# Kernel tuning notes

Hardware: AMD Instinct MI355X
Metric: run time of the kernel (lower is better)

## Reference

```python
import jax, jax.numpy as jnp
import numpy as np


def setup_inputs() -> dict:
    key = jax.random.key(0)
    ks = jax.random.split(key, 5)
    B, S, H = 4, 4096, 512
    std = 1.0 / np.sqrt(H)
    x = jax.random.normal(ks[0], (B, S, H), dtype=jnp.float32)
    relative_pos = jax.random.normal(ks[1], (B, S, H), dtype=jnp.float32)
    Wq = jax.random.normal(ks[2], (H, H), dtype=jnp.float32) * std
    Wk = jax.random.normal(ks[3], (H, H), dtype=jnp.float32) * std
    Wv = jax.random.normal(ks[4], (H, H), dtype=jnp.float32) * std
    bq = jnp.zeros((H,), dtype=jnp.float32)
    bk = jnp.zeros((H,), dtype=jnp.float32)
    bv = jnp.zeros((H,), dtype=jnp.float32)
    return {"x": x, "relative_pos": relative_pos, "Wq": Wq, "bq": bq,
            "Wk": Wk, "bk": bk, "Wv": Wv, "bv": bv}


def reference(x, relative_pos, Wq, bq, Wk, bk, Wv, bv):
    H = x.shape[-1]
    scale = jnp.sqrt(jnp.asarray(H, dtype=x.dtype))
    # torch Linear: y = x @ W^T + b
    Q = jnp.einsum('bsh,oh->bso', x, Wq) + bq
    K = jnp.einsum('bsh,oh->bso', x, Wk) + bk
    V = jnp.einsum('bsh,oh->bso', x, Wv) + bv
    Kr = jnp.einsum('bsh,oh->bso', relative_pos, Wk) + bk
    # two score terms, each [B,S,S]
    scores = (jnp.einsum('bqd,bkd->bqk', Q, K) +
              jnp.einsum('bqd,bkd->bqk', Q, Kr)) / scale
    weights = jax.nn.softmax(scores, axis=-1)
    return jnp.einsum('bqk,bkd->bqd', weights, V)
```

## Files before the change

kernel.cpp:

```cpp
#include <hip/hip_runtime.h>
#include <stdint.h>

typedef __attribute__((ext_vector_type(8))) short bf16x8;
typedef __attribute__((ext_vector_type(4))) float f32x4;

#define AS1 __attribute__((address_space(1)))
#define AS3 __attribute__((address_space(3)))

__device__ __forceinline__ void gl2lds16(const void* g, void* l) {
    __builtin_amdgcn_global_load_lds((const AS1 void*)g, (AS3 void*)l, 16, 0, 0);
}

__device__ __forceinline__ unsigned short f2bf(float f) {
    uint32_t u = __builtin_bit_cast(uint32_t, f);
    uint32_t r = (u + 0x7fffu + ((u >> 16) & 1u)) >> 16;
    return (unsigned short)r;
}

constexpr int S = 4096;
constexpr int H = 512;
constexpr size_t OFF_XB  = 0;
constexpr size_t OFF_SB  = 16777216;
constexpr size_t OFF_WQB = 33554432;
constexpr size_t OFF_WKB = 34078720;
constexpr size_t OFF_WVB = 34603008;
constexpr size_t OFF_BQK = 35127296;
constexpr size_t OFF_QB  = 35131392;
constexpr size_t OFF_K2B = OFF_QB  + 16777216;
constexpr size_t OFF_VTB = OFF_K2B + 16777216;
constexpr size_t OFF_PB  = OFF_VTB + 16777216;
constexpr size_t OFF_L   = OFF_PB  + 134217728;

__global__ __launch_bounds__(256) void prep_x(const float* __restrict__ x,
                                              const float* __restrict__ rp,
                                              unsigned short* __restrict__ xb,
                                              unsigned short* __restrict__ sb) {
    const int i = (blockIdx.x * 256 + threadIdx.x) * 4;
    float4 xv = *(const float4*)(x + i);
    float4 rv = *(const float4*)(rp + i);
    uint2 xo, so;
    xo.x = (uint32_t)f2bf(xv.x) | ((uint32_t)f2bf(xv.y) << 16);
    xo.y = (uint32_t)f2bf(xv.z) | ((uint32_t)f2bf(xv.w) << 16);
    so.x = (uint32_t)f2bf(xv.x + rv.x) | ((uint32_t)f2bf(xv.y + rv.y) << 16);
    so.y = (uint32_t)f2bf(xv.z + rv.z) | ((uint32_t)f2bf(xv.w + rv.w) << 16);
    *(uint2*)(xb + i) = xo;
    *(uint2*)(sb + i) = so;
}

__global__ __launch_bounds__(256) void prep_w(const float* __restrict__ wq,
                                              const float* __restrict__ wk,
                                              const float* __restrict__ wv,
                                              const float* __restrict__ bq,
                                              const float* __restrict__ bk,
                                              unsigned short* __restrict__ wqb,
                                              unsigned short* __restrict__ wkb,
                                              unsigned short* __restrict__ wvb,
                                              float* __restrict__ bqk,
                                              float* __restrict__ lrow) {
    const int t = blockIdx.x * 256 + threadIdx.x;
    const int i = t * 4;
    float4 q = *(const float4*)(wq + i);
    float4 k = *(const float4*)(wk + i);
    float4 v = *(const float4*)(wv + i);
    uint2 o;
    o.x = (uint32_t)f2bf(q.x) | ((uint32_t)f2bf(q.y) << 16);
    o.y = (uint32_t)f2bf(q.z) | ((uint32_t)f2bf(q.w) << 16);
    *(uint2*)(wqb + i) = o;
    o.x = (uint32_t)f2bf(k.x) | ((uint32_t)f2bf(k.y) << 16);
    o.y = (uint32_t)f2bf(k.z) | ((uint32_t)f2bf(k.w) << 16);
    *(uint2*)(wkb + i) = o;
    o.x = (uint32_t)f2bf(v.x) | ((uint32_t)f2bf(v.y) << 16);
    o.y = (uint32_t)f2bf(v.z) | ((uint32_t)f2bf(v.w) << 16);
    *(uint2*)(wvb + i) = o;
    if (t < 128) {
        *(float4*)(bqk + t * 4) = *(const float4*)(bq + t * 4);
    } else if (t < 256) {
        const int u = t - 128;
        float4 b = *(const float4*)(bk + u * 4);
        *(float4*)(bqk + 512 + u * 4) = make_float4(2.f * b.x, 2.f * b.y, 2.f * b.z, 2.f * b.w);
    }
    if (t < 4096) {
        *(float4*)(lrow + t * 4) = make_float4(0.f, 0.f, 0.f, 0.f);
    }
}

template <int MODE, int SWZ>
__global__ __launch_bounds__(256, 2)
void gemm_bt(const unsigned short* __restrict__ Abase,
             const unsigned short* __restrict__ Bbase,
             void* __restrict__ Cbase,
             int M, int N, int K,
             long long sAz, long long sBz, long long sCz,
             const float* __restrict__ bias_n, long long sBNz,
             const float* __restrict__ bias_m,
             float scale,
             float* __restrict__ rowdiv, long long sRz)
{
    int bx = blockIdx.x, by = blockIdx.y, bz = blockIdx.z;
    if (SWZ) {
        const int gx = gridDim.x, gy = gridDim.y;
        const int id  = bx + gx * (by + gridDim.y * bz);
        const int xcd = id & 7;
        const int k   = id >> 3;
        const int kg  = k / gx;
        bx = k - kg * gx;
        const int g = xcd + 8 * kg;
        const int gz = g / gy;
        by = g - gz * gy;
        bz = gz;
    }
    const int z = bz;
    const unsigned short* A  = Abase + (size_t)z * (size_t)sAz;
    const unsigned short* Bm = Bbase + (size_t)z * (size_t)sBz;
    const int bn = bx * 128;
    const int bm = by * 128;

    __shared__ __align__(16) unsigned short As[128 * 32];
    __shared__ __align__(16) unsigned short Bs[128 * 32];

    const int tid  = threadIdx.x;
    const int wave = tid >> 6;
    const int lane = tid & 63;
    const int lm   = lane & 15;
    const int quad = lane >> 4;
    const int wm   = (wave >> 1) * 64;
    const int wn   = (wave & 1) * 64;

    const int r0 = tid >> 2;
    const int p0 = tid & 3;
    unsigned short* AsW0 = As + wave * 512;
    unsigned short* AsW1 = As + 2048 + wave * 512;
    unsigned short* BsW0 = Bs + wave * 512;
    unsigned short* BsW1 = Bs + 2048 + wave * 512;

    f32x4 acc[4][4] = {};

    for (int k0 = 0; k0 < K; k0 += 32) {
        const unsigned short* Ap = A  + (size_t)(bm + r0) * K + k0 + p0 * 8;
        const unsigned short* Bp = Bm + (size_t)(bn + r0) * K + k0 + p0 * 8;
        __syncthreads();
        gl2lds16(Ap, AsW0);
        gl2lds16(Ap + (size_t)64 * K, AsW1);
        gl2lds16(Bp, BsW0);
        gl2lds16(Bp + (size_t)64 * K, BsW1);
        __syncthreads();

        bf16x8 af[4], bfr[4];
        #pragma unroll
        for (int t = 0; t < 4; t++) {
            af[t]  = *(const bf16x8*)(As + (wm + t * 16 + lm) * 32 + quad * 8);
            bfr[t] = *(const bf16x8*)(Bs + (wn + t * 16 + lm) * 32 + quad * 8);
        }
        #pragma unroll
        for (int mt = 0; mt < 4; mt++)
            #pragma unroll
            for (int nt = 0; nt < 4; nt++)
                acc[mt][nt] = __builtin_amdgcn_mfma_f32_16x16x32_bf16(af[mt], bfr[nt], acc[mt][nt], 0, 0, 0);
    }

    if (MODE == 0) {
        unsigned short* C = (unsigned short*)Cbase + (size_t)z * (size_t)sCz;
        const float* bn_ptr = bias_n ? bias_n + (size_t)z * (size_t)sBNz : nullptr;
        #pragma unroll
        for (int mt = 0; mt < 4; mt++) {
            #pragma unroll
            for (int i = 0; i < 4; i++) {
                const int row = bm + wm + mt * 16 + quad * 4 + i;
                const float badd = bias_m ? bias_m[row] : 0.0f;
                const size_t rb = (size_t)row * (size_t)N;
                #pragma unroll
                for (int nt = 0; nt < 4; nt++) {
                    const int col = bn + wn + nt * 16 + lm;
                    float v = acc[mt][nt][i] * scale + badd;
                    if (bn_ptr) v += bn_ptr[col];
                    C[rb + col] = f2bf(v);
                }
            }
        }
    } else if (MODE == 1) {
        float* C = (float*)Cbase + (size_t)z * (size_t)sCz;
        const float* rd = rowdiv + (size_t)z * (size_t)sRz;
        #pragma unroll
        for (int mt = 0; mt < 4; mt++) {
            #pragma unroll
            for (int i = 0; i < 4; i++) {
                const int row = bm + wm + mt * 16 + quad * 4 + i;
                const float inv = 1.0f / rd[row];
                const size_t rb = (size_t)row * (size_t)N;
                #pragma unroll
                for (int nt = 0; nt < 4; nt++) {
                    const int col = bn + wn + nt * 16 + lm;
                    C[rb + col] = acc[mt][nt][i] * inv;
                }
            }
        }
    } else {
        unsigned short* C = (unsigned short*)Cbase + (size_t)z * (size_t)sCz;
        float* lr = rowdiv + (size_t)z * (size_t)sRz;
        #pragma unroll
        for (int mt = 0; mt < 4; mt++) {
            #pragma unroll
            for (int i = 0; i < 4; i++) {
                const int row = bm + wm + mt * 16 + quad * 4 + i;
                const size_t rb = (size_t)row * (size_t)N;
                float rsum = 0.f;
                #pragma unroll
                for (int nt = 0; nt < 4; nt++) {
                    const int col = bn + wn + nt * 16 + lm;
                    float p = __expf(acc[mt][nt][i] * scale);
                    rsum += p;
                    C[rb + col] = f2bf(p);
                }
                rsum += __shfl_xor(rsum, 1);
                rsum += __shfl_xor(rsum, 2);
                rsum += __shfl_xor(rsum, 4);
                rsum += __shfl_xor(rsum, 8);
                if (lm == 0) atomicAdd(lr + row, rsum);
            }
        }
    }
}

extern "C" void kernel_launch(void* const* d_in, const int* in_sizes, int n_in,
                              void* d_out, int out_size, void* d_ws, size_t ws_size,
                              hipStream_t stream) {
    const float* x  = (const float*)d_in[0];
    const float* rp = (const float*)d_in[1];
    const float* Wq = (const float*)d_in[2];
    const float* bq = (const float*)d_in[3];
    const float* Wk = (const float*)d_in[4];
    const float* bk = (const float*)d_in[5];
    const float* Wv = (const float*)d_in[6];
    const float* bv = (const float*)d_in[7];

    char* ws = (char*)d_ws;
    unsigned short* xb  = (unsigned short*)(ws + OFF_XB);
    unsigned short* sb  = (unsigned short*)(ws + OFF_SB);
    unsigned short* wqb = (unsigned short*)(ws + OFF_WQB);
    unsigned short* wkb = (unsigned short*)(ws + OFF_WKB);
    unsigned short* wvb = (unsigned short*)(ws + OFF_WVB);
    float*          bqk = (float*)(ws + OFF_BQK);
    unsigned short* qb  = (unsigned short*)(ws + OFF_QB);
    unsigned short* k2b = (unsigned short*)(ws + OFF_K2B);
    unsigned short* vtb = (unsigned short*)(ws + OFF_VTB);
    unsigned short* pb  = (unsigned short*)(ws + OFF_PB);
    float*          lrow = (float*)(ws + OFF_L);

    prep_x<<<8192, 256, 0, stream>>>(x, rp, xb, sb);
    prep_w<<<256, 256, 0, stream>>>(Wq, Wk, Wv, bq, bk, wqb, wkb, wvb, bqk, lrow);

    gemm_bt<0, 1><<<dim3(4, 128, 2), 256, 0, stream>>>(xb, wqb, qb, 16384, 512, 512,
                                                       8388608, 262144, 8388608,
                                                       bqk, 512, nullptr, 1.0f, nullptr, 0);
    gemm_bt<0, 0><<<dim3(32, 4, 4), 256, 0, stream>>>(wvb, xb, vtb, 512, 4096, 512,
                                                      0, (long long)S * H, (long long)S * H,
                                                      nullptr, 0, bv, 1.0f, nullptr, 0);
    gemm_bt<2, 0><<<dim3(32, 32, 4), 256, 0, stream>>>(qb, k2b, pb, 4096, 4096, 512,
                                                       (long long)S * H, (long long)S * H,
                                                       (long long)S * S,
                                                       nullptr, 0, nullptr, 0.044194173824159216f,
                                                       lrow, 4096);
    gemm_bt<1, 1><<<dim3(4, 32, 4), 256, 0, stream>>>(pb, vtb, d_out, 4096, 512, 4096,
                                                      (long long)S * S, (long long)S * H,
                                                      (long long)S * H,
                                                      nullptr, 0, nullptr, 1.0f, lrow, 4096);
}
```

Before: 370.4 us.

## Stage score-exp tile through LDS for coalesced stores; narrow PV GEMM tile

The exp/score GEMM epilogue now writes its bf16 probability tile into LDS in two 64-row halves, then stores it to global memory with 16-byte coalesced rows instead of scattered 2-byte stores. That launch also gains the XCD-aware block swizzle. The final P·V GEMM uses a 64-wide N tile with 4 blocks per CU, doubling its grid so more blocks run at once, at the cost of less B-tile reuse per block. The staged epilogue adds extra barriers and LDS traffic.

```diff
diff --git a/kernel.cpp b/kernel.cpp
--- a/kernel.cpp
+++ b/kernel.cpp
@@ -84,8 +84,8 @@
     }
 }
 
-template <int MODE, int SWZ>
-__global__ __launch_bounds__(256, 2)
+template <int MODE, int SWZ, int TN, int MINW>
+__global__ __launch_bounds__(256, MINW)
 void gemm_bt(const unsigned short* __restrict__ Abase,
              const unsigned short* __restrict__ Bbase,
              void* __restrict__ Cbase,
@@ -96,6 +96,7 @@
              float scale,
              float* __restrict__ rowdiv, long long sRz)
 {
+    constexpr int NT = TN / 32;
     int bx = blockIdx.x, by = blockIdx.y, bz = blockIdx.z;
     if (SWZ) {
         const int gx = gridDim.x, gy = gridDim.y;
@@ -112,11 +113,13 @@
     const int z = bz;
     const unsigned short* A  = Abase + (size_t)z * (size_t)sAz;
     const unsigned short* Bm = Bbase + (size_t)z * (size_t)sBz;
-    const int bn = bx * 128;
+    const int bn = bx * TN;
     const int bm = by * 128;
 
-    __shared__ __align__(16) unsigned short As[128 * 32];
-    __shared__ __align__(16) unsigned short Bs[128 * 32];
+    constexpr int SMEM_BYTES = (MODE == 2) ? (64 * 136 * 2) : ((128 + TN) * 32 * 2);
+    __shared__ __align__(16) char smem[SMEM_BYTES];
+    unsigned short* As = (unsigned short*)smem;
+    unsigned short* Bs = (unsigned short*)(smem + 128 * 32 * 2);
 
     const int tid  = threadIdx.x;
     const int wave = tid >> 6;
@@ -124,7 +127,7 @@
     const int lm   = lane & 15;
     const int quad = lane >> 4;
     const int wm   = (wave >> 1) * 64;
-    const int wn   = (wave & 1) * 64;
+    const int wn   = (wave & 1) * (TN / 2);
 
     const int r0 = tid >> 2;
     const int p0 = tid & 3;
@@ -133,7 +136,7 @@
     unsigned short* BsW0 = Bs + wave * 512;
     unsigned short* BsW1 = Bs + 2048 + wave * 512;
 
-    f32x4 acc[4][4] = {};
+    f32x4 acc[4][NT] = {};
 
     for (int k0 = 0; k0 < K; k0 += 32) {
         const unsigned short* Ap = A  + (size_t)(bm + r0) * K + k0 + p0 * 8;
@@ -142,19 +145,20 @@
         gl2lds16(Ap, AsW0);
         gl2lds16(Ap + (size_t)64 * K, AsW1);
         gl2lds16(Bp, BsW0);
-        gl2lds16(Bp + (size_t)64 * K, BsW1);
+        if (TN == 128) gl2lds16(Bp + (size_t)64 * K, BsW1);
         __syncthreads();
 
-        bf16x8 af[4], bfr[4];
-        #pragma unroll
-        for (int t = 0; t < 4; t++) {
+        bf16x8 af[4], bfr[NT];
+        #pragma unroll
+        for (int t = 0; t < 4; t++)
             af[t]  = *(const bf16x8*)(As + (wm + t * 16 + lm) * 32 + quad * 8);
+        #pragma unroll
+        for (int t = 0; t < NT; t++)
             bfr[t] = *(const bf16x8*)(Bs + (wn + t * 16 + lm) * 32 + quad * 8);
-        }
         #pragma unroll
         for (int mt = 0; mt < 4; mt++)
             #pragma unroll
-            for (int nt = 0; nt < 4; nt++)
+            for (int nt = 0; nt < NT; nt++)
                 acc[mt][nt] = __builtin_amdgcn_mfma_f32_16x16x32_bf16(af[mt], bfr[nt], acc[mt][nt], 0, 0, 0);
     }
 
@@ -169,7 +173,7 @@
                 const float badd = bias_m ? bias_m[row] : 0.0f;
                 const size_t rb = (size_t)row * (size_t)N;
                 #pragma unroll
-                for (int nt = 0; nt < 4; nt++) {
+                for (int nt = 0; nt < NT; nt++) {
                     const int col = bn + wn + nt * 16 + lm;
                     float v = acc[mt][nt][i] * scale + badd;
                     if (bn_ptr) v += bn_ptr[col];
@@ -188,7 +192,7 @@
                 const float inv = 1.0f / rd[row];
                 const size_t rb = (size_t)row * (size_t)N;
                 #pragma unroll
-                for (int nt = 0; nt < 4; nt++) {
+                for (int nt = 0; nt < NT; nt++) {
                     const int col = bn + wn + nt * 16 + lm;
                     C[rb + col] = acc[mt][nt][i] * inv;
                 }
@@ -197,25 +201,39 @@
     } else {
         unsigned short* C = (unsigned short*)Cbase + (size_t)z * (size_t)sCz;
         float* lr = rowdiv + (size_t)z * (size_t)sRz;
-        #pragma unroll
-        for (int mt = 0; mt < 4; mt++) {
-            #pragma unroll
-            for (int i = 0; i < 4; i++) {
-                const int row = bm + wm + mt * 16 + quad * 4 + i;
-                const size_t rb = (size_t)row * (size_t)N;
-                float rsum = 0.f;
+        unsigned short* Ct = (unsigned short*)smem;
+        #pragma unroll
+        for (int h = 0; h < 2; h++) {
+            __syncthreads();
+            if ((wave >> 1) == h) {
                 #pragma unroll
-                for (int nt = 0; nt < 4; nt++) {
-                    const int col = bn + wn + nt * 16 + lm;
-                    float p = __expf(acc[mt][nt][i] * scale);
-                    rsum += p;
-                    C[rb + col] = f2bf(p);
+                for (int mt = 0; mt < 4; mt++) {
+                    #pragma unroll
+                    for (int i = 0; i < 4; i++) {
+                        const int r = mt * 16 + quad * 4 + i;
+                        const int row = bm + wm + r;
+                        float rsum = 0.f;
+                        #pragma unroll
+                        for (int nt = 0; nt < NT; nt++) {
+                            float p = __expf(acc[mt][nt][i] * scale);
+                            rsum += p;
+                            Ct[r * 136 + wn + nt * 16 + lm] = f2bf(p);
+                        }
+                        rsum += __shfl_xor(rsum, 1);
+                        rsum += __shfl_xor(rsum, 2);
+                        rsum += __shfl_xor(rsum, 4);
+                        rsum += __shfl_xor(rsum, 8);
+                        if (lm == 0) atomicAdd(lr + row, rsum);
+                    }
                 }
-                rsum += __shfl_xor(rsum, 1);
-                rsum += __shfl_xor(rsum, 2);
-                rsum += __shfl_xor(rsum, 4);
-                rsum += __shfl_xor(rsum, 8);
-                if (lm == 0) atomicAdd(lr + row, rsum);
+            }
+            __syncthreads();
+            #pragma unroll
+            for (int j = 0; j < 4; j++) {
+                const int r   = (tid >> 4) + 16 * j;
+                const int c16 = tid & 15;
+                uint4 vv = *(const uint4*)(Ct + r * 136 + c16 * 8);
+                *(uint4*)(C + (size_t)(bm + 64 * h + r) * (size_t)N + bn + c16 * 8) = vv;
             }
         }
     }
@@ -249,19 +267,21 @@
     prep_x<<<8192, 256, 0, stream>>>(x, rp, xb, sb);
     prep_w<<<256, 256, 0, stream>>>(Wq, Wk, Wv, bq, bk, wqb, wkb, wvb, bqk, lrow);
 
-    gemm_bt<0, 1><<<dim3(4, 128, 2), 256, 0, stream>>>(xb, wqb, qb, 16384, 512, 512,
-                                                       8388608, 262144, 8388608,
-                                                       bqk, 512, nullptr, 1.0f, nullptr, 0);
-    gemm_bt<0, 0><<<dim3(32, 4, 4), 256, 0, stream>>>(wvb, xb, vtb, 512, 4096, 512,
-                                                      0, (long long)S * H, (long long)S * H,
-                                                      nullptr, 0, bv, 1.0f, nullptr, 0);
-    gemm_bt<2, 0><<<dim3(32, 32, 4), 256, 0, stream>>>(qb, k2b, pb, 4096, 4096, 512,
-                                                       (long long)S * H, (long long)S * H,
-                                                       (long long)S * S,
-                                                       nullptr, 0, nullptr, 0.044194173824159216f,
-                                                       lrow, 4096);
-    gemm_bt<1, 1><<<dim3(4, 32, 4), 256, 0, stream>>>(pb, vtb, d_out, 4096, 512, 4096,
-                                                      (long long)S * S, (long long)S * H,
-                                                      (long long)S * H,
-                                                      nullptr, 0, nullptr, 1.0f, lrow, 4096);
-}
+    gemm_bt<0, 1, 128, 2><<<dim3(4, 128, 2), 256, 0, stream>>>(
+        xb, wqb, qb, 16384, 512, 512,
+        8388608, 262144, 8388608,
+        bqk, 512, nullptr, 1.0f, nullptr, 0);
+    gemm_bt<0, 0, 128, 2><<<dim3(32, 4, 4), 256, 0, stream>>>(
+        wvb, xb, vtb, 512, 4096, 512,
+        0, (long long)S * H, (long long)S * H,
+        nullptr, 0, bv, 1.0f, nullptr, 0);
+    gemm_bt<2, 1, 128, 2><<<dim3(32, 32, 4), 256, 0, stream>>>(
+        qb, k2b, pb, 4096, 4096, 512,
+        (long long)S * H, (long long)S * H, (long long)S * S,
+        nullptr, 0, nullptr, 0.044194173824159216f,
+        lrow, 4096);
+    gemm_bt<1, 1, 64, 4><<<dim3(8, 32, 4), 256, 0, stream>>>(
+        pb, vtb, d_out, 4096, 512, 4096,
+        (long long)S * S, (long long)S * H, (long long)S * H,
+        nullptr, 0, nullptr, 1.0f, lrow, 4096);
+}
```

New measurement: 407.5 us. 1.1x slower.
